# Optimization experiments

Measured on AMD Instinct MI355X. Metric: run time of the kernel, lower is better.

The kernel has to match this reference:

```python
import jax, jax.numpy as jnp
import numpy as np


def setup_inputs() -> dict:
    key = jax.random.key(0)
    k1, k2, k3, k4, k5, k6 = jax.random.split(key, 6)
    B, N, D, H = 32, 4096, 256, 256
    return {
        "queries": jax.random.normal(k1, (B, N, D), dtype=jnp.float32),
        "keys": jax.random.normal(k2, (B, N, D), dtype=jnp.float32),
        "values": jax.random.normal(k3, (B, N, D), dtype=jnp.float32),
        "Wq": jax.random.normal(k4, (H, D), dtype=jnp.float32) * (1.0 / np.sqrt(D)),
        "Wk": jax.random.normal(k5, (H, D), dtype=jnp.float32) * (1.0 / np.sqrt(D)),
        "Wv": jax.random.normal(k6, (1, H), dtype=jnp.float32) * (1.0 / np.sqrt(H)),
    }


def reference(queries, keys, values, Wq, Wk, Wv):
    # Project queries and keys to hidden dim (torch Linear weight is [out, in])
    q = jnp.einsum('bnd,hd->bnh', queries, Wq)   # [B, N, H]
    k = jnp.einsum('bnd,hd->bnh', keys, Wk)      # [B, N, H]
    features = jnp.tanh(q + k)                   # [B, N, H]
    scores = jnp.einsum('bnh,oh->bno', features, Wv)  # [B, N, 1]
    alpha = jax.nn.softmax(scores, axis=1)       # softmax over N
    # dropout p=0 -> identity
    aggr_max = jnp.argmax(alpha, axis=1)         # [B, 1]
    out = jnp.sum(alpha * values, axis=1)        # [B, D]
    return (out, aggr_max)
```

## Files before the change

kernel.cpp:

```cpp
#include <hip/hip_runtime.h>

#define Bb 32
#define Nn 4096
#define Dd 256
#define Hh 256
#define NCH 32
#define CHUNK 128

typedef __attribute__((ext_vector_type(8))) _Float16 half8;
typedef __attribute__((ext_vector_type(4))) float f32x4;

__device__ __forceinline__ float fast_tanhf(float x) {
    float e = __expf(2.0f * x);
    return 1.0f - 2.0f / (e + 1.0f);
}

__device__ __forceinline__ half8 cvt8(f32x4 v0, f32x4 v1) {
    half8 h;
    h[0] = (_Float16)v0.x; h[1] = (_Float16)v0.y;
    h[2] = (_Float16)v0.z; h[3] = (_Float16)v0.w;
    h[4] = (_Float16)v1.x; h[5] = (_Float16)v1.y;
    h[6] = (_Float16)v1.z; h[7] = (_Float16)v1.w;
    return h;
}

__global__ __launch_bounds__(256) void prep_w_kernel(
    const float* __restrict__ Wq, const float* __restrict__ Wk,
    _Float16* __restrict__ Wf)
{
    const int g = blockIdx.x * 256 + threadIdx.x;
    const int s = g >> 10;
    const int j = (g >> 6) & 15;
    const int l = g & 63;
    const int n = j * 16 + (l & 15);
    const int k = s * 32 + (l >> 4) * 8;
    const float* src = (k < 256) ? (Wq + n * 256 + k) : (Wk + n * 256 + (k - 256));
    const f32x4 v0 = *(const f32x4*)src;
    const f32x4 v1 = *(const f32x4*)(src + 4);
    *(half8*)&Wf[(size_t)g * 8] = cvt8(v0, v1);
}

__global__ __launch_bounds__(256, 3) void scores_tile_kernel(
    const float* __restrict__ Q, const float* __restrict__ Kmat,
    const _Float16* __restrict__ Wf,
    const float* __restrict__ Wv, float* __restrict__ scores)
{
    __shared__ _Float16 Abuf[2][4096];
    __shared__ float red[4][64];

    const int tid = threadIdx.x;
    const int lane = tid & 63;
    const int wave = tid >> 6;
    const size_t row0 = (size_t)blockIdx.x * 64;

    f32x4 acc[4][4];
#pragma unroll
    for (int m = 0; m < 4; ++m)
#pragma unroll
        for (int n = 0; n < 4; ++n) acc[m][n] = (f32x4){0.f, 0.f, 0.f, 0.f};

    float wv[4];
#pragma unroll
    for (int n = 0; n < 4; ++n) wv[n] = Wv[wave * 64 + n * 16 + (lane & 15)];

    const int srow = ((tid >> 6) << 4) + (tid & 15);
    const int skf  = ((tid >> 4) & 3) * 8;

    f32x4 a0, a1, a2, a3;
    half8 BB[8];

    auto issue_a = [&](int s) {
        const float* base = (s < 4)
            ? (Q    + (row0 + srow) * Dd + s * 64)
            : (Kmat + (row0 + srow) * Dd + (s - 4) * 64);
        const float* p0 = base + skf;
        const float* p1 = base + 32 + skf;
        a0 = *(const f32x4*)p0; a1 = *(const f32x4*)(p0 + 4);
        a2 = *(const f32x4*)p1; a3 = *(const f32x4*)(p1 + 4);
    };
    auto store_a = [&](int buf) {
        *(half8*)&Abuf[buf][tid * 8] = cvt8(a0, a1);
        *(half8*)&Abuf[buf][(tid + 256) * 8] = cvt8(a2, a3);
    };
    auto issue_b = [&](int s) {
#pragma unroll
        for (int kk = 0; kk < 2; ++kk)
#pragma unroll
            for (int n = 0; n < 4; ++n)
                BB[kk * 4 + n] = *(const half8*)(Wf +
                    ((size_t)((s * 2 + kk) * 16 + wave * 4 + n) * 64 + lane) * 8);
    };
    auto cluster = [&](int buf) {
        __builtin_amdgcn_s_setprio(1);
#pragma unroll
        for (int kk = 0; kk < 2; ++kk)
#pragma unroll
            for (int m = 0; m < 4; ++m) {
                const half8 a = *(const half8*)&Abuf[buf][(kk * 256 + m * 64 + lane) * 8];
#pragma unroll
                for (int n = 0; n < 4; ++n)
                    acc[m][n] = __builtin_amdgcn_mfma_f32_16x16x32_f16(a, BB[kk * 4 + n], acc[m][n], 0, 0, 0);
            }
        __builtin_amdgcn_s_setprio(0);
    };

    issue_a(0);
    store_a(0);
    __syncthreads();

    for (int s = 0; s < 8; ++s) {
        issue_b(s);
        if (s < 7) issue_a(s + 1);
        cluster(s & 1);
        if (s < 7) store_a((s + 1) & 1);
        __syncthreads();
    }

    const int q = lane >> 4;
    float rp[4][4];
#pragma unroll
    for (int m = 0; m < 4; ++m)
#pragma unroll
        for (int r = 0; r < 4; ++r) {
            float v = 0.f;
#pragma unroll
            for (int n = 0; n < 4; ++n)
                v += wv[n] * fast_tanhf(acc[m][n][r]);
            rp[m][r] = v;
        }
#pragma unroll
    for (int mask = 1; mask <= 8; mask <<= 1)
#pragma unroll
        for (int m = 0; m < 4; ++m)
#pragma unroll
            for (int r = 0; r < 4; ++r)
                rp[m][r] += __shfl_xor(rp[m][r], mask, 64);

    if ((lane & 15) == 0) {
#pragma unroll
        for (int m = 0; m < 4; ++m)
#pragma unroll
            for (int r = 0; r < 4; ++r)
                red[wave][m * 16 + q * 4 + r] = rp[m][r];
    }
    __syncthreads();
    if (tid < 64)
        scores[row0 + tid] = (red[0][tid] + red[1][tid]) + (red[2][tid] + red[3][tid]);
}

#define MAXC 64
__global__ __launch_bounds__(256) void softmax_reduce_kernel(
    const float* __restrict__ scores,
    const float* __restrict__ Qg, const float* __restrict__ Kg,
    const float* __restrict__ Wq, const float* __restrict__ Wk,
    const float* __restrict__ Wv,
    float* __restrict__ mbuf, float* __restrict__ zbuf, float* __restrict__ out)
{
    __shared__ float sv[256];
    __shared__ int si[256];
    __shared__ double dred[256];
    __shared__ int cand[MAXC];
    __shared__ int cnt;
    const int b = blockIdx.x;
    const int tid = threadIdx.x;
    const float* sc = scores + (size_t)b * Nn;

    float best = -1e30f; int bi = 0;
    for (int j = 0; j < Nn / 256; ++j) {
        const int n = tid + j * 256;
        const float v = sc[n];
        if (v > best) { best = v; bi = n; }
    }
    sv[tid] = best; si[tid] = bi;
    __syncthreads();
    for (int off = 128; off > 0; off >>= 1) {
        if (tid < off) {
            const float v2 = sv[tid + off]; const int i2 = si[tid + off];
            if (v2 > sv[tid] || (v2 == sv[tid] && i2 < si[tid])) { sv[tid] = v2; si[tid] = i2; }
        }
        __syncthreads();
    }
    const float m = sv[0];
    int amax = si[0];
    __syncthreads();

    float ssum = 0.f;
    for (int j = 0; j < Nn / 256; ++j) ssum += __expf(sc[tid + j * 256] - m);
    sv[tid] = ssum;
    __syncthreads();
    for (int off = 128; off > 0; off >>= 1) {
        if (tid < off) sv[tid] += sv[tid + off];
        __syncthreads();
    }
    const float Z = sv[0];
    __syncthreads();

    if (tid == 0) cnt = 0;
    __syncthreads();
    const float tau = 0.02f;
    for (int j = 0; j < Nn / 256; ++j) {
        const int n = tid + j * 256;
        if (sc[n] >= m - tau) {
            const int p = atomicAdd(&cnt, 1);
            if (p < MAXC) cand[p] = n;
        }
    }
    __syncthreads();
    const int ncand = (cnt < MAXC) ? cnt : MAXC;
    if (ncand > 1) {
        double bestv = -1e300; int besti = 0x7fffffff;
        for (int c = 0; c < ncand; ++c) {
            const int n = cand[c];
            const float* qr = Qg + ((size_t)b * Nn + n) * Dd;
            const float* kr = Kg + ((size_t)b * Nn + n) * Dd;
            const float* wqr = Wq + tid * Dd;
            const float* wkr = Wk + tid * Dd;
            double accd = 0.0;
            for (int k2 = 0; k2 < Dd; ++k2)
                accd += (double)qr[k2] * (double)wqr[k2] + (double)kr[k2] * (double)wkr[k2];
            dred[tid] = (double)Wv[tid] * tanh(accd);
            __syncthreads();
            for (int off = 128; off > 0; off >>= 1) {
                if (tid < off) dred[tid] += dred[tid + off];
                __syncthreads();
            }
            const double s_c = dred[0];
            __syncthreads();
            if (s_c > bestv || (s_c == bestv && n < besti)) { bestv = s_c; besti = n; }
        }
        amax = besti;
    }

    if (tid == 0) {
        mbuf[b] = m;
        zbuf[b] = Z;
        out[(size_t)Bb * Dd + b] = (float)amax;
    }
}

__global__ __launch_bounds__(256) void partial_kernel(
    const float* __restrict__ V, const float* __restrict__ scores,
    const float* __restrict__ mbuf, float* __restrict__ part)
{
    __shared__ float e[CHUNK];
    const int c = blockIdx.x;
    const int b = blockIdx.y;
    const int tid = threadIdx.x;
    const float m = mbuf[b];
    if (tid < CHUNK)
        e[tid] = __expf(scores[(size_t)b * Nn + (size_t)c * CHUNK + tid] - m);
    __syncthreads();

    const float* vp = V + ((size_t)b * Nn + (size_t)c * CHUNK) * Dd + tid;
    float a0 = 0.f, a1 = 0.f, a2 = 0.f, a3 = 0.f;
    for (int n = 0; n < CHUNK; n += 4) {
        a0 = fmaf(e[n + 0], vp[(size_t)(n + 0) * Dd], a0);
        a1 = fmaf(e[n + 1], vp[(size_t)(n + 1) * Dd], a1);
        a2 = fmaf(e[n + 2], vp[(size_t)(n + 2) * Dd], a2);
        a3 = fmaf(e[n + 3], vp[(size_t)(n + 3) * Dd], a3);
    }
    part[((size_t)b * NCH + c) * Dd + tid] = ((a0 + a1) + (a2 + a3));
}

__global__ __launch_bounds__(256) void finalize_kernel(
    const float* __restrict__ part, const float* __restrict__ zbuf,
    float* __restrict__ out)
{
    const int b = blockIdx.x;
    const int tid = threadIdx.x;
    float s = 0.f;
#pragma unroll
    for (int c = 0; c < NCH; ++c) s += part[((size_t)b * NCH + c) * Dd + tid];
    out[(size_t)b * Dd + tid] = s / zbuf[b];
}

extern "C" void kernel_launch(void* const* d_in, const int* in_sizes, int n_in,
                              void* d_out, int out_size, void* d_ws, size_t ws_size,
                              hipStream_t stream) {
    const float* Q  = (const float*)d_in[0];
    const float* K  = (const float*)d_in[1];
    const float* V  = (const float*)d_in[2];
    const float* Wq = (const float*)d_in[3];
    const float* Wk = (const float*)d_in[4];
    const float* Wv = (const float*)d_in[5];
    float* out = (float*)d_out;

    char* wsb = (char*)d_ws;
    _Float16* Wf  = (_Float16*)(wsb);
    float* scores = (float*)(wsb + 262144);
    float* mbuf   = (float*)(wsb + 786432);
    float* zbuf   = (float*)(wsb + 786432 + 128);
    float* part   = (float*)(wsb + 786432 + 256);

    prep_w_kernel<<<dim3(64), dim3(256), 0, stream>>>(Wq, Wk, Wf);
    scores_tile_kernel<<<dim3((Bb * Nn) / 64), dim3(256), 0, stream>>>(Q, K, Wf, Wv, scores);
    softmax_reduce_kernel<<<dim3(Bb), dim3(256), 0, stream>>>(scores, Q, K, Wq, Wk, Wv, mbuf, zbuf, out);
    partial_kernel<<<dim3(NCH, Bb), dim3(256), 0, stream>>>(V, scores, mbuf, part);
    finalize_kernel<<<dim3(Bb), dim3(256), 0, stream>>>(part, zbuf, out);
}
```

Measured before the change: 149.4 us.

## Stream Q/K tiles to LDS via global_load_lds DMA instead of register staging

Replaces the register-staged load, fp16 convert and LDS store of the Q/K tiles with direct global-to-LDS 16-byte DMA loads into an fp32 LDS buffer. The fp32-to-fp16 conversion moves to the MFMA loop, where tiles are read back from LDS. This is meant to cut VGPR pressure and the store latency in the pipelined loop. In exchange it doubles LDS footprint and LDS read bandwidth, and adds convert instructions in the compute cluster.

```diff
diff --git a/kernel.cpp b/kernel.cpp
--- a/kernel.cpp
+++ b/kernel.cpp
@@ -9,6 +9,10 @@
 
 typedef __attribute__((ext_vector_type(8))) _Float16 half8;
 typedef __attribute__((ext_vector_type(4))) float f32x4;
+
+#define GLDS16(gp, lp) __builtin_amdgcn_global_load_lds( \
+    (const __attribute__((address_space(1))) unsigned int*)(gp), \
+    (__attribute__((address_space(3))) unsigned int*)(lp), 16, 0, 0)
 
 __device__ __forceinline__ float fast_tanhf(float x) {
     float e = __expf(2.0f * x);
@@ -40,12 +44,12 @@
     *(half8*)&Wf[(size_t)g * 8] = cvt8(v0, v1);
 }
 
-__global__ __launch_bounds__(256, 3) void scores_tile_kernel(
+__global__ __launch_bounds__(256, 3) void scores_dma_kernel(
     const float* __restrict__ Q, const float* __restrict__ Kmat,
     const _Float16* __restrict__ Wf,
     const float* __restrict__ Wv, float* __restrict__ scores)
 {
-    __shared__ _Float16 Abuf[2][4096];
+    __shared__ float Abuf[2][4096];
     __shared__ float red[4][64];
 
     const int tid = threadIdx.x;
@@ -63,25 +67,18 @@
 #pragma unroll
     for (int n = 0; n < 4; ++n) wv[n] = Wv[wave * 64 + n * 16 + (lane & 15)];
 
-    const int srow = ((tid >> 6) << 4) + (tid & 15);
-    const int skf  = ((tid >> 4) & 3) * 8;
-
-    f32x4 a0, a1, a2, a3;
+    int eoff[4];
+#pragma unroll
+    for (int j = 0; j < 4; ++j) {
+        const int i = wave * 4 + j;
+        const int kk = i >> 3;
+        const int m  = (i >> 1) & 3;
+        const int row_local = m * 16 + ((lane >> 1) & 15);
+        const int kloc = kk * 32 + ((i & 1) * 2 + (lane >> 5)) * 8 + (lane & 1) * 4;
+        eoff[j] = row_local * Dd + kloc;
+    }
+
     half8 BB[8];
-
-    auto issue_a = [&](int s) {
-        const float* base = (s < 4)
-            ? (Q    + (row0 + srow) * Dd + s * 64)
-            : (Kmat + (row0 + srow) * Dd + (s - 4) * 64);
-        const float* p0 = base + skf;
-        const float* p1 = base + 32 + skf;
-        a0 = *(const f32x4*)p0; a1 = *(const f32x4*)(p0 + 4);
-        a2 = *(const f32x4*)p1; a3 = *(const f32x4*)(p1 + 4);
-    };
-    auto store_a = [&](int buf) {
-        *(half8*)&Abuf[buf][tid * 8] = cvt8(a0, a1);
-        *(half8*)&Abuf[buf][(tid + 256) * 8] = cvt8(a2, a3);
-    };
     auto issue_b = [&](int s) {
 #pragma unroll
         for (int kk = 0; kk < 2; ++kk)
@@ -90,13 +87,24 @@
                 BB[kk * 4 + n] = *(const half8*)(Wf +
                     ((size_t)((s * 2 + kk) * 16 + wave * 4 + n) * 64 + lane) * 8);
     };
+    auto dma_a = [&](int buf, int s) {
+        const float* base = (s < 4) ? (Q    + row0 * Dd + s * 64)
+                                    : (Kmat + row0 * Dd + (s - 4) * 64);
+        char* lbase = (char*)&Abuf[buf][0] + wave * 4096;
+#pragma unroll
+        for (int j = 0; j < 4; ++j)
+            GLDS16(base + eoff[j], lbase + j * 1024);
+    };
     auto cluster = [&](int buf) {
         __builtin_amdgcn_s_setprio(1);
 #pragma unroll
         for (int kk = 0; kk < 2; ++kk)
 #pragma unroll
             for (int m = 0; m < 4; ++m) {
-                const half8 a = *(const half8*)&Abuf[buf][(kk * 256 + m * 64 + lane) * 8];
+                const float* fp = &Abuf[buf][(kk * 256 + m * 64 + lane) * 8];
+                const f32x4 lo = *(const f32x4*)fp;
+                const f32x4 hi = *(const f32x4*)(fp + 4);
+                const half8 a = cvt8(lo, hi);
 #pragma unroll
                 for (int n = 0; n < 4; ++n)
                     acc[m][n] = __builtin_amdgcn_mfma_f32_16x16x32_f16(a, BB[kk * 4 + n], acc[m][n], 0, 0, 0);
@@ -104,15 +112,13 @@
         __builtin_amdgcn_s_setprio(0);
     };
 
-    issue_a(0);
-    store_a(0);
+    dma_a(0, 0);
     __syncthreads();
 
     for (int s = 0; s < 8; ++s) {
         issue_b(s);
-        if (s < 7) issue_a(s + 1);
+        if (s < 7) dma_a((s + 1) & 1, s + 1);
         cluster(s & 1);
-        if (s < 7) store_a((s + 1) & 1);
         __syncthreads();
     }
 
@@ -293,7 +299,7 @@
     float* part   = (float*)(wsb + 786432 + 256);
 
     prep_w_kernel<<<dim3(64), dim3(256), 0, stream>>>(Wq, Wk, Wf);
-    scores_tile_kernel<<<dim3((Bb * Nn) / 64), dim3(256), 0, stream>>>(Q, K, Wf, Wv, scores);
+    scores_dma_kernel<<<dim3((Bb * Nn) / 64), dim3(256), 0, stream>>>(Q, K, Wf, Wv, scores);
     softmax_reduce_kernel<<<dim3(Bb), dim3(256), 0, stream>>>(scores, Q, K, Wq, Wk, Wv, mbuf, zbuf, out);
     partial_kernel<<<dim3(NCH, Bb), dim3(256), 0, stream>>>(V, scores, mbuf, part);
     finalize_kernel<<<dim3(Bb), dim3(256), 0, stream>>>(part, zbuf, out);
```

New measurement: 146.3 us. 1.02x faster.
